# Optimization experiments

Measured on AMD Instinct MI355X. Metric: run time of the kernel, lower is better.

## Reference

```python
import jax, jax.numpy as jnp
import numpy as np

N_NODES = 50000


def _sage_conv(x, src, dst, Wl, Wr, bl, num_nodes):
    # PyG SAGEConv (mean aggr): out = lin_l(mean_{j in N(i)} x_j) + lin_r(x_i)
    # messages flow src -> dst
    agg = jax.ops.segment_sum(x[src], dst, num_segments=num_nodes)          # [N, F]
    deg = jax.ops.segment_sum(jnp.ones_like(dst, dtype=x.dtype), dst,
                              num_segments=num_nodes)                       # [N]
    agg = agg / jnp.maximum(deg, 1.0)[:, None]
    return agg @ Wl + bl + x @ Wr


def setup_inputs() -> dict:
    key = jax.random.key(0)
    ks = jax.random.split(key, 9)
    F_in, H, C, E = 256, 256, 40, 800000
    s = lambda fan: 1.0 / np.sqrt(fan)
    x = jax.random.normal(ks[0], (N_NODES, F_in), dtype=jnp.float32)
    edge_index = jax.random.randint(ks[1], (2, E), 0, N_NODES, dtype=jnp.int32)
    W1l = jax.random.normal(ks[2], (F_in, H), dtype=jnp.float32) * s(F_in)
    W1r = jax.random.normal(ks[3], (F_in, H), dtype=jnp.float32) * s(F_in)
    b1 = jnp.zeros((H,), dtype=jnp.float32)
    W2l = jax.random.normal(ks[4], (H, C), dtype=jnp.float32) * s(H)
    W2r = jax.random.normal(ks[5], (H, C), dtype=jnp.float32) * s(H)
    b2 = jnp.zeros((C,), dtype=jnp.float32)
    Q = jax.random.normal(ks[6], (E // 2, C), dtype=jnp.float32) * s(E // 2)
    return {"x": x, "edge_index": edge_index, "W1l": W1l, "b1": b1,
            "W1r": W1r, "W2l": W2l, "b2": b2, "W2r": W2r, "Q": Q}


def reference(x, edge_index, W1l, b1, W1r, W2l, b2, W2r, Q):
    # Eval mode: F.dropout with training=False is identity.
    src, dst = edge_index[0], edge_index[1]
    h = _sage_conv(x, src, dst, W1l, W1r, b1, N_NODES)
    h = jax.nn.elu(h)
    out = _sage_conv(h, src, dst, W2l, W2r, b2, N_NODES)
    return (out, Q)
```

## Files before the change

### kernel.cpp

```cpp
#include <hip/hip_runtime.h>
#include <hip/hip_bf16.h>
#include <cstddef>

#define N_NODES 50000
#define M_PAD 50048

typedef __attribute__((ext_vector_type(8))) short short8;
typedef __attribute__((ext_vector_type(4))) float floatx4;

__device__ inline unsigned short f2bf(float f) {
    union { float f; unsigned u; } v; v.f = f;
    unsigned r = v.u + 0x7fff + ((v.u >> 16) & 1);
    return (unsigned short)(r >> 16);
}
__device__ inline float bfbits_lo(unsigned u) {
    union { unsigned u; float f; } v; v.u = u << 16; return v.f;
}
__device__ inline float bfbits_hi(unsigned u) {
    union { unsigned u; float f; } v; v.u = u & 0xffff0000u; return v.f;
}

__device__ inline void gload16(const void* g, void* l) {
    __builtin_amdgcn_global_load_lds(
        (const __attribute__((address_space(1))) unsigned int*)g,
        (__attribute__((address_space(3))) unsigned int*)l, 16, 0, 0);
}

__global__ __launch_bounds__(256) void prep_count(
    const float* __restrict__ x,
    const float* __restrict__ W1l, const float* __restrict__ W1r,
    const float* __restrict__ W2l, const float* __restrict__ W2r,
    unsigned short* __restrict__ Abuf, unsigned short* __restrict__ B1t,
    unsigned short* __restrict__ B2t,
    const int* __restrict__ dst, int* __restrict__ deg, int E) {
    int b = blockIdx.x;
    int tid = threadIdx.x;
    if (b < 6250) {
        int i = b * 256 + tid;
        int row = i >> 5;
        int c8 = i & 31;
        const float4* xp = reinterpret_cast<const float4*>(x + (size_t)row * 256 + c8 * 8);
        float4 v0 = xp[0], v1 = xp[1];
        uint4 o;
        o.x = (unsigned)f2bf(v0.x) | ((unsigned)f2bf(v0.y) << 16);
        o.y = (unsigned)f2bf(v0.z) | ((unsigned)f2bf(v0.w) << 16);
        o.z = (unsigned)f2bf(v1.x) | ((unsigned)f2bf(v1.y) << 16);
        o.w = (unsigned)f2bf(v1.z) | ((unsigned)f2bf(v1.w) << 16);
        *reinterpret_cast<uint4*>(Abuf + (size_t)row * 512 + 256 + c8 * 8) = o;
    } else if (b < 6250 + 512) {
        int idx = (b - 6250) * 256 + tid;
        int n = idx >> 9, k = idx & 511;
        float v = (k < 256) ? W1l[(size_t)k * 256 + n] : W1r[(size_t)(k - 256) * 256 + n];
        B1t[(size_t)n * 512 + k] = f2bf(v);
    } else if (b < 6842) {
        int idx = (b - 6762) * 256 + tid;
        int n = idx >> 8, k = idx & 255;
        float v = (n < 40) ? W2l[(size_t)k * 40 + n] : W2r[(size_t)k * 40 + (n - 40)];
        B2t[(size_t)n * 256 + k] = f2bf(v);
    } else {
        int base = (b - 6842) * 256 + tid;
        for (int e = base; e < E; e += 1024 * 256)
            atomicAdd(&deg[dst[e]], 1);
    }
}

__global__ __launch_bounds__(256) void scan1_kernel(const int* __restrict__ deg,
                                                    int* __restrict__ blocksums, int n) {
    __shared__ int s[256];
    int t = threadIdx.x;
    int i = blockIdx.x * 256 + t;
    s[t] = (i < n) ? deg[i] : 0;
    __syncthreads();
    for (int off = 128; off > 0; off >>= 1) {
        if (t < off) s[t] += s[t + off];
        __syncthreads();
    }
    if (t == 0) blocksums[blockIdx.x] = s[0];
}

__global__ __launch_bounds__(256) void scan2_kernel(const int* __restrict__ blocksums,
                                                    int* __restrict__ blockoff, int nb) {
    __shared__ int s[256];
    int t = threadIdx.x;
    s[t] = (t < nb) ? blocksums[t] : 0;
    __syncthreads();
    for (int off = 1; off < 256; off <<= 1) {
        int u = (t >= off) ? s[t - off] : 0;
        __syncthreads();
        s[t] += u;
        __syncthreads();
    }
    if (t < nb) blockoff[t] = (t == 0) ? 0 : s[t - 1];
}

__global__ __launch_bounds__(256) void scan3_kernel(const int* __restrict__ deg,
                                                    const int* __restrict__ blockoff,
                                                    int* __restrict__ rowptr,
                                                    float* __restrict__ inv_deg,
                                                    int n, int E) {
    __shared__ int s[256];
    int t = threadIdx.x;
    int i = blockIdx.x * 256 + t;
    int v = (i < n) ? deg[i] : 0;
    s[t] = v;
    __syncthreads();
    for (int off = 1; off < 256; off <<= 1) {
        int u = (t >= off) ? s[t - off] : 0;
        __syncthreads();
        s[t] += u;
        __syncthreads();
    }
    if (i < n) {
        rowptr[i] = s[t] - v + blockoff[blockIdx.x];
        inv_deg[i] = 1.0f / (float)(v > 1 ? v : 1);
    }
    if (blockIdx.x == 0 && t == 0) rowptr[n] = E;
}

__global__ void fill_q(const int* __restrict__ src, const int* __restrict__ dst,
                       const int* __restrict__ rowptr, int* __restrict__ cnt,
                       int* __restrict__ csr, int E,
                       const float4* __restrict__ Qsrc, float4* __restrict__ Qdst,
                       int nQ4) {
    if ((int)blockIdx.x >= 1024) {
        int idx = (blockIdx.x - 1024) * 256 + threadIdx.x;
        for (int i = idx; i < nQ4; i += 1024 * 256) Qdst[i] = Qsrc[i];
        return;
    }
    for (int e = blockIdx.x * blockDim.x + threadIdx.x; e < E; e += 1024 * 256) {
        int d = dst[e];
        int p = rowptr[d] + atomicAdd(&cnt[d], 1);
        csr[p] = src[e];
    }
}

__global__ __launch_bounds__(256) void aggregate1(
    const unsigned short* __restrict__ Abuf, const int* __restrict__ rowptr,
    const int* __restrict__ csr, const float* __restrict__ inv_deg,
    unsigned short* __restrict__ AbufOut, int N) {
    int node = blockIdx.x * 4 + (threadIdx.x >> 6);
    if (node >= N) return;
    int lane = threadIdx.x & 63;
    int half = lane >> 5;
    int dlane = lane & 31;
    const unsigned short* base = Abuf + 256 + (size_t)dlane * 8;
    float a0 = 0.f, a1 = 0.f, a2 = 0.f, a3 = 0.f;
    float a4 = 0.f, a5 = 0.f, a6 = 0.f, a7 = 0.f;
    int beg = rowptr[node], end = rowptr[node + 1];
    int k = beg + half;
    for (; k + 7 < end; k += 8) {
        int j0 = csr[k], j1 = csr[k + 2], j2 = csr[k + 4], j3 = csr[k + 6];
        uint4 v0 = *reinterpret_cast<const uint4*>(base + (size_t)j0 * 512);
        uint4 v1 = *reinterpret_cast<const uint4*>(base + (size_t)j1 * 512);
        uint4 v2 = *reinterpret_cast<const uint4*>(base + (size_t)j2 * 512);
        uint4 v3 = *reinterpret_cast<const uint4*>(base + (size_t)j3 * 512);
        a0 += bfbits_lo(v0.x); a1 += bfbits_hi(v0.x); a2 += bfbits_lo(v0.y); a3 += bfbits_hi(v0.y);
        a4 += bfbits_lo(v0.z); a5 += bfbits_hi(v0.z); a6 += bfbits_lo(v0.w); a7 += bfbits_hi(v0.w);
        a0 += bfbits_lo(v1.x); a1 += bfbits_hi(v1.x); a2 += bfbits_lo(v1.y); a3 += bfbits_hi(v1.y);
        a4 += bfbits_lo(v1.z); a5 += bfbits_hi(v1.z); a6 += bfbits_lo(v1.w); a7 += bfbits_hi(v1.w);
        a0 += bfbits_lo(v2.x); a1 += bfbits_hi(v2.x); a2 += bfbits_lo(v2.y); a3 += bfbits_hi(v2.y);
        a4 += bfbits_lo(v2.z); a5 += bfbits_hi(v2.z); a6 += bfbits_lo(v2.w); a7 += bfbits_hi(v2.w);
        a0 += bfbits_lo(v3.x); a1 += bfbits_hi(v3.x); a2 += bfbits_lo(v3.y); a3 += bfbits_hi(v3.y);
        a4 += bfbits_lo(v3.z); a5 += bfbits_hi(v3.z); a6 += bfbits_lo(v3.w); a7 += bfbits_hi(v3.w);
    }
    for (; k < end; k += 2) {
        int j = csr[k];
        uint4 v = *reinterpret_cast<const uint4*>(base + (size_t)j * 512);
        a0 += bfbits_lo(v.x); a1 += bfbits_hi(v.x); a2 += bfbits_lo(v.y); a3 += bfbits_hi(v.y);
        a4 += bfbits_lo(v.z); a5 += bfbits_hi(v.z); a6 += bfbits_lo(v.w); a7 += bfbits_hi(v.w);
    }
    a0 += __shfl_xor(a0, 32, 64); a1 += __shfl_xor(a1, 32, 64);
    a2 += __shfl_xor(a2, 32, 64); a3 += __shfl_xor(a3, 32, 64);
    a4 += __shfl_xor(a4, 32, 64); a5 += __shfl_xor(a5, 32, 64);
    a6 += __shfl_xor(a6, 32, 64); a7 += __shfl_xor(a7, 32, 64);
    if (half == 0) {
        float s = inv_deg[node];
        uint4 w;
        w.x = (unsigned)f2bf(a0 * s) | ((unsigned)f2bf(a1 * s) << 16);
        w.y = (unsigned)f2bf(a2 * s) | ((unsigned)f2bf(a3 * s) << 16);
        w.z = (unsigned)f2bf(a4 * s) | ((unsigned)f2bf(a5 * s) << 16);
        w.w = (unsigned)f2bf(a6 * s) | ((unsigned)f2bf(a7 * s) << 16);
        *reinterpret_cast<uint4*>(AbufOut + (size_t)node * 512 + dlane * 8) = w;
    }
}

__global__ __launch_bounds__(256) void gemm1_mfma(
    const unsigned short* __restrict__ Abuf,
    const unsigned short* __restrict__ B1t,
    const float* __restrict__ bias,
    unsigned short* __restrict__ H,
    int M) {
    __shared__ unsigned short As[2][64 * 64];
    __shared__ unsigned short Bs[2][128 * 64];
    int tid = threadIdx.x;
    int row0 = blockIdx.x * 64;
    int bn = blockIdx.y;
    int wid = tid >> 6, lane = tid & 63;
    int wm = (wid >> 1) * 32;
    int wn = (wid & 1) * 64;
    int fr = lane & 15, fq = lane >> 4;

    int lrow8 = lane >> 3;
    int gco = ((lane & 7) ^ lrow8) * 8;
    const unsigned short* gA0 = Abuf + (size_t)(row0 + wid * 16 + 0 + lrow8) * 512 + gco;
    const unsigned short* gA1 = Abuf + (size_t)(row0 + wid * 16 + 8 + lrow8) * 512 + gco;
    const unsigned short* gB0 = B1t + (size_t)(bn * 128 + wid * 32 + 0  + lrow8) * 512 + gco;
    const unsigned short* gB1 = B1t + (size_t)(bn * 128 + wid * 32 + 8  + lrow8) * 512 + gco;
    const unsigned short* gB2 = B1t + (size_t)(bn * 128 + wid * 32 + 16 + lrow8) * 512 + gco;
    const unsigned short* gB3 = B1t + (size_t)(bn * 128 + wid * 32 + 24 + lrow8) * 512 + gco;

    floatx4 acc[2][4] = {};

    #define STAGE(buf, k0)                                       \
        gload16(gA0 + (k0), &As[buf][(wid * 16 + 0) * 64]);      \
        gload16(gA1 + (k0), &As[buf][(wid * 16 + 8) * 64]);      \
        gload16(gB0 + (k0), &Bs[buf][(wid * 32 + 0) * 64]);      \
        gload16(gB1 + (k0), &Bs[buf][(wid * 32 + 8) * 64]);      \
        gload16(gB2 + (k0), &Bs[buf][(wid * 32 + 16) * 64]);     \
        gload16(gB3 + (k0), &Bs[buf][(wid * 32 + 24) * 64]);

    #define COMPUTE(buf)                                                                  \
        {                                                                                 \
            _Pragma("unroll")                                                             \
            for (int kc = 0; kc < 2; ++kc) {                                              \
                short8 af[2], bfr[4];                                                     \
                _Pragma("unroll")                                                         \
                for (int mi = 0; mi < 2; ++mi) {                                          \
                    int row = wm + mi * 16 + fr;                                          \
                    af[mi] = *reinterpret_cast<const short8*>(                            \
                        &As[buf][row * 64 + (((kc * 4 + fq) ^ (fr & 7)) * 8)]);           \
                }                                                                         \
                _Pragma("unroll")                                                         \
                for (int ni = 0; ni < 4; ++ni) {                                          \
                    int row = wn + ni * 16 + fr;                                          \
                    bfr[ni] = *reinterpret_cast<const short8*>(                           \
                        &Bs[buf][row * 64 + (((kc * 4 + fq) ^ (fr & 7)) * 8)]);           \
                }                                                                         \
                _Pragma("unroll")                                                         \
                for (int mi = 0; mi < 2; ++mi)                                            \
                    _Pragma("unroll")                                                     \
                    for (int ni = 0; ni < 4; ++ni)                                        \
                        acc[mi][ni] = __builtin_amdgcn_mfma_f32_16x16x32_bf16(            \
                            af[mi], bfr[ni], acc[mi][ni], 0, 0, 0);                       \
            }                                                                             \
        }

    STAGE(0, 0);
    __syncthreads();
    int cur = 0;
    #pragma unroll 1
    for (int t = 0; t < 7; ++t) {
        STAGE(cur ^ 1, (t + 1) * 64);
        COMPUTE(cur);
        __syncthreads();
        cur ^= 1;
    }
    COMPUTE(cur);
    #undef STAGE
    #undef COMPUTE

    #pragma unroll
    for (int ni = 0; ni < 4; ++ni) {
        int gcol = bn * 128 + wn + ni * 16 + fr;
        float bb = bias[gcol];
        #pragma unroll
        for (int mi = 0; mi < 2; ++mi) {
            #pragma unroll
            for (int r = 0; r < 4; ++r) {
                int grow = row0 + wm + mi * 16 + fq * 4 + r;
                float t = acc[mi][ni][r] + bb;
                t = (t > 0.f) ? t : expm1f(t);
                H[(size_t)grow * 256 + gcol] = f2bf(t);
            }
        }
    }
}

__global__ __launch_bounds__(256) void gemm2_mfma(
    const unsigned short* __restrict__ Hb,
    const unsigned short* __restrict__ B2t,
    const float* __restrict__ b2,
    unsigned short* __restrict__ Plb,
    float* __restrict__ Pr,
    int M) {
    __shared__ unsigned short Bsm[80 * 256];
    __shared__ unsigned short As[2][64 * 64];
    int tid = threadIdx.x;
    int row0 = blockIdx.x * 64;
    int wid = tid >> 6, lane = tid & 63;
    int wm = wid * 16;
    int fr = lane & 15, fq = lane >> 4;

    for (int c = tid; c < 2560; c += 256) {
        int n = c >> 5, ci = c & 31;
        short8 v = *reinterpret_cast<const short8*>(B2t + (size_t)n * 256 + ci * 8);
        *reinterpret_cast<short8*>(&Bsm[n * 256 + ((ci ^ (n & 7)) * 8)]) = v;
    }

    int lrow8 = lane >> 3;
    int gco = ((lane & 7) ^ lrow8) * 8;
    const unsigned short* gA0 = Hb + (size_t)(row0 + wid * 16 + 0 + lrow8) * 256 + gco;
    const unsigned short* gA1 = Hb + (size_t)(row0 + wid * 16 + 8 + lrow8) * 256 + gco;

    floatx4 acc[5] = {};

    #define STAGE2(buf, k0)                                      \
        gload16(gA0 + (k0), &As[buf][(wid * 16 + 0) * 64]);      \
        gload16(gA1 + (k0), &As[buf][(wid * 16 + 8) * 64]);

    #define COMPUTE2(buf, k0)                                                             \
        {                                                                                 \
            _Pragma("unroll")                                                             \
            for (int kc = 0; kc < 2; ++kc) {                                              \
                short8 af;                                                                \
                {                                                                         \
                    int row = wm + fr;                                                    \
                    af = *reinterpret_cast<const short8*>(                                \
                        &As[buf][row * 64 + (((kc * 4 + fq) ^ (fr & 7)) * 8)]);           \
                }                                                                         \
                _Pragma("unroll")                                                         \
                for (int ni = 0; ni < 5; ++ni) {                                          \
                    int n = ni * 16 + fr;                                                 \
                    int c = ((k0) >> 3) + kc * 4 + fq;                                    \
                    short8 bfr = *reinterpret_cast<const short8*>(                        \
                        &Bsm[n * 256 + ((c ^ (n & 7)) * 8)]);                             \
                    acc[ni] = __builtin_amdgcn_mfma_f32_16x16x32_bf16(                    \
                        af, bfr, acc[ni], 0, 0, 0);                                       \
                }                                                                         \
            }                                                                             \
        }

    STAGE2(0, 0);
    __syncthreads();
    int cur = 0;
    #pragma unroll 1
    for (int t = 0; t < 3; ++t) {
        STAGE2(cur ^ 1, (t + 1) * 64);
        COMPUTE2(cur, t * 64);
        __syncthreads();
        cur ^= 1;
    }
    COMPUTE2(cur, 192);
    #undef STAGE2
    #undef COMPUTE2

    #pragma unroll
    for (int r = 0; r < 4; ++r) {
        int grow = row0 + wm + fq * 4 + r;
        if (grow < M) {
            #pragma unroll
            for (int ni = 0; ni < 5; ++ni) {
                int col = ni * 16 + fr;
                float v = acc[ni][r];
                if (col < 40)
                    Plb[(size_t)grow * 40 + col] = f2bf(v);
                else
                    Pr[(size_t)grow * 40 + (col - 40)] = v + b2[col - 40];
            }
        }
    }
}

__global__ __launch_bounds__(256) void final_kernel(
    const unsigned short* __restrict__ Plb, const float* __restrict__ Pr,
    const int* __restrict__ rowptr, const int* __restrict__ csr,
    const float* __restrict__ inv_deg, float* __restrict__ out, int N) {
    int wv = blockIdx.x * 4 + (threadIdx.x >> 6);
    int node = wv * 2 + ((threadIdx.x >> 5) & 1);
    if (node >= N) return;
    int lane = threadIdx.x & 31;
    if (lane >= 20) return;
    float s0 = 0.f, s1 = 0.f;
    int beg = rowptr[node], end = rowptr[node + 1];
    int k = beg;
    for (; k + 4 <= end; k += 4) {
        unsigned v0 = *reinterpret_cast<const unsigned*>(Plb + (size_t)csr[k]     * 40 + lane * 2);
        unsigned v1 = *reinterpret_cast<const unsigned*>(Plb + (size_t)csr[k + 1] * 40 + lane * 2);
        unsigned v2 = *reinterpret_cast<const unsigned*>(Plb + (size_t)csr[k + 2] * 40 + lane * 2);
        unsigned v3 = *reinterpret_cast<const unsigned*>(Plb + (size_t)csr[k + 3] * 40 + lane * 2);
        s0 += bfbits_lo(v0) + bfbits_lo(v1) + bfbits_lo(v2) + bfbits_lo(v3);
        s1 += bfbits_hi(v0) + bfbits_hi(v1) + bfbits_hi(v2) + bfbits_hi(v3);
    }
    for (; k < end; ++k) {
        unsigned v = *reinterpret_cast<const unsigned*>(Plb + (size_t)csr[k] * 40 + lane * 2);
        s0 += bfbits_lo(v);
        s1 += bfbits_hi(v);
    }
    float inv = inv_deg[node];
    float2 pr = *reinterpret_cast<const float2*>(Pr + (size_t)node * 40 + lane * 2);
    float2 o;
    o.x = s0 * inv + pr.x;
    o.y = s1 * inv + pr.y;
    *reinterpret_cast<float2*>(out + (size_t)node * 40 + lane * 2) = o;
}


extern "C" void kernel_launch(void* const* d_in, const int* in_sizes, int n_in,
                              void* d_out, int out_size, void* d_ws, size_t ws_size,
                              hipStream_t stream) {
    const float* x   = (const float*)d_in[0];
    const int*   ei  = (const int*)d_in[1];
    const float* W1l = (const float*)d_in[2];
    const float* b1  = (const float*)d_in[3];
    const float* W1r = (const float*)d_in[4];
    const float* W2l = (const float*)d_in[5];
    const float* b2  = (const float*)d_in[6];
    const float* W2r = (const float*)d_in[7];
    const float* Q   = (const float*)d_in[8];
    const int E = in_sizes[1] / 2;
    const int N = N_NODES;
    const int* src = ei;
    const int* dst = ei + E;
    const int NB = (N + 255) / 256;

    unsigned short* Abuf = (unsigned short*)d_ws;
    unsigned short* h    = Abuf + (size_t)M_PAD * 512;
    unsigned short* B1t  = h + (size_t)M_PAD * 256;
    unsigned short* B2t  = B1t + 256 * 512;
    unsigned short* Plb  = B2t + 80 * 256;
    float* Pr      = (float*)(Plb + (size_t)N * 40 + 32);
    float* inv_deg = Pr + (size_t)N * 40;
    int*   deg     = (int*)(inv_deg + N);
    int*   cnt     = deg + N;
    int*   rowptr  = cnt + N;
    int*   blocksums = rowptr + N + 1;
    int*   blockoff  = blocksums + NB;
    int*   csr     = blockoff + NB;

    float* out = (float*)d_out;

    hipMemsetAsync(deg, 0, sizeof(int) * 2 * (size_t)N, stream);
    prep_count<<<6842 + 1024, 256, 0, stream>>>(x, W1l, W1r, W2l, W2r,
                                                Abuf, B1t, B2t, dst, deg, E);
    scan1_kernel<<<NB, 256, 0, stream>>>(deg, blocksums, N);
    scan2_kernel<<<1, 256, 0, stream>>>(blocksums, blockoff, NB);
    scan3_kernel<<<NB, 256, 0, stream>>>(deg, blockoff, rowptr, inv_deg, N, E);

    const int nQ4 = in_sizes[8] / 4;
    fill_q<<<2048, 256, 0, stream>>>(src, dst, rowptr, cnt, csr, E,
                                     (const float4*)Q,
                                     (float4*)(out + (size_t)N * 40), nQ4);

    aggregate1<<<(N + 3) / 4, 256, 0, stream>>>(Abuf, rowptr, csr, inv_deg, Abuf, N);
    gemm1_mfma<<<dim3(M_PAD / 64, 2), 256, 0, stream>>>(Abuf, B1t, b1, h, N);
    gemm2_mfma<<<M_PAD / 64, 256, 0, stream>>>(h, B2t, b2, Plb, Pr, N);
    final_kernel<<<(N + 7) / 8, 256, 0, stream>>>(Plb, Pr, rowptr, csr, inv_deg, out, N);
}
```

Before: 255.7 us.

## Record per-edge rank during degree count; move Q copy into gemm1 grid

The degree-counting pass now stores each edge's atomicAdd return value as its rank within its destination row. The CSR fill then becomes a plain scatter with no second round of atomics, and the cnt array and its memset go away. The Q copy moves out of the fill kernel into an extra grid slice of gemm1 so it overlaps with GEMM work. The cost is an extra E-sized int array that is written and then read back.

```diff
diff --git a/kernel.cpp b/kernel.cpp
--- a/kernel.cpp
+++ b/kernel.cpp
@@ -32,7 +32,8 @@
     const float* __restrict__ W2l, const float* __restrict__ W2r,
     unsigned short* __restrict__ Abuf, unsigned short* __restrict__ B1t,
     unsigned short* __restrict__ B2t,
-    const int* __restrict__ dst, int* __restrict__ deg, int E) {
+    const int* __restrict__ dst, int* __restrict__ deg, int* __restrict__ erank,
+    int E) {
     int b = blockIdx.x;
     int tid = threadIdx.x;
     if (b < 6250) {
@@ -60,7 +61,7 @@
     } else {
         int base = (b - 6842) * 256 + tid;
         for (int e = base; e < E; e += 1024 * 256)
-            atomicAdd(&deg[dst[e]], 1);
+            erank[e] = atomicAdd(&deg[dst[e]], 1);
     }
 }
 
@@ -117,21 +118,11 @@
     if (blockIdx.x == 0 && t == 0) rowptr[n] = E;
 }
 
-__global__ void fill_q(const int* __restrict__ src, const int* __restrict__ dst,
-                       const int* __restrict__ rowptr, int* __restrict__ cnt,
-                       int* __restrict__ csr, int E,
-                       const float4* __restrict__ Qsrc, float4* __restrict__ Qdst,
-                       int nQ4) {
-    if ((int)blockIdx.x >= 1024) {
-        int idx = (blockIdx.x - 1024) * 256 + threadIdx.x;
-        for (int i = idx; i < nQ4; i += 1024 * 256) Qdst[i] = Qsrc[i];
-        return;
-    }
-    for (int e = blockIdx.x * blockDim.x + threadIdx.x; e < E; e += 1024 * 256) {
-        int d = dst[e];
-        int p = rowptr[d] + atomicAdd(&cnt[d], 1);
-        csr[p] = src[e];
-    }
+__global__ void fill_kernel(const int* __restrict__ src, const int* __restrict__ dst,
+                            const int* __restrict__ erank, const int* __restrict__ rowptr,
+                            int* __restrict__ csr, int E) {
+    for (int e = blockIdx.x * blockDim.x + threadIdx.x; e < E; e += gridDim.x * blockDim.x)
+        csr[rowptr[dst[e]] + erank[e]] = src[e];
 }
 
 __global__ __launch_bounds__(256) void aggregate1(
@@ -189,12 +180,19 @@
     const unsigned short* __restrict__ B1t,
     const float* __restrict__ bias,
     unsigned short* __restrict__ H,
-    int M) {
+    int M,
+    const float4* __restrict__ Qsrc, float4* __restrict__ Qdst, int nQ4) {
     __shared__ unsigned short As[2][64 * 64];
     __shared__ unsigned short Bs[2][128 * 64];
     int tid = threadIdx.x;
+    int bn = blockIdx.y;
+    if (bn == 2) {
+        int idx = blockIdx.x * 256 + tid;
+        int stride = gridDim.x * 256;
+        for (int i = idx; i < nQ4; i += stride) Qdst[i] = Qsrc[i];
+        return;
+    }
     int row0 = blockIdx.x * 64;
-    int bn = blockIdx.y;
     int wid = tid >> 6, lane = tid & 63;
     int wm = (wid >> 1) * 32;
     int wn = (wid & 1) * 64;
@@ -421,28 +419,29 @@
     float* Pr      = (float*)(Plb + (size_t)N * 40 + 32);
     float* inv_deg = Pr + (size_t)N * 40;
     int*   deg     = (int*)(inv_deg + N);
-    int*   cnt     = deg + N;
-    int*   rowptr  = cnt + N;
+    int*   rowptr  = deg + N;
     int*   blocksums = rowptr + N + 1;
     int*   blockoff  = blocksums + NB;
     int*   csr     = blockoff + NB;
+    int*   erank   = csr + E;
 
     float* out = (float*)d_out;
 
-    hipMemsetAsync(deg, 0, sizeof(int) * 2 * (size_t)N, stream);
+    hipMemsetAsync(deg, 0, sizeof(int) * (size_t)N, stream);
     prep_count<<<6842 + 1024, 256, 0, stream>>>(x, W1l, W1r, W2l, W2r,
-                                                Abuf, B1t, B2t, dst, deg, E);
+                                                Abuf, B1t, B2t, dst, deg, erank, E);
     scan1_kernel<<<NB, 256, 0, stream>>>(deg, blocksums, N);
     scan2_kernel<<<1, 256, 0, stream>>>(blocksums, blockoff, NB);
     scan3_kernel<<<NB, 256, 0, stream>>>(deg, blockoff, rowptr, inv_deg, N, E);
 
+    fill_kernel<<<1024, 256, 0, stream>>>(src, dst, erank, rowptr, csr, E);
+
+    aggregate1<<<(N + 3) / 4, 256, 0, stream>>>(Abuf, rowptr, csr, inv_deg, Abuf, N);
+
     const int nQ4 = in_sizes[8] / 4;
-    fill_q<<<2048, 256, 0, stream>>>(src, dst, rowptr, cnt, csr, E,
-                                     (const float4*)Q,
-                                     (float4*)(out + (size_t)N * 40), nQ4);
-
-    aggregate1<<<(N + 3) / 4, 256, 0, stream>>>(Abuf, rowptr, csr, inv_deg, Abuf, N);
-    gemm1_mfma<<<dim3(M_PAD / 64, 2), 256, 0, stream>>>(Abuf, B1t, b1, h, N);
+    gemm1_mfma<<<dim3(M_PAD / 64, 3), 256, 0, stream>>>(
+        Abuf, B1t, b1, h, N, (const float4*)Q, (float4*)(out + (size_t)N * 40), nQ4);
+
     gemm2_mfma<<<M_PAD / 64, 256, 0, stream>>>(h, B2t, b2, Plb, Pr, N);
     final_kernel<<<(N + 7) / 8, 256, 0, stream>>>(Plb, Pr, rowptr, csr, inv_deg, out, N);
 }
```

Result: faster. 232.7 us (-9.0%).
